# Kernel tuning notes

Hardware: AMD Instinct MI355X
Metric: run time of the kernel (lower is better)

Reference implementation:

```python
import jax, jax.numpy as jnp
import numpy as np

EMBED_DIM = 1024
NUM_HEADS = 16
D_K = EMBED_DIM // NUM_HEADS


def setup_inputs() -> dict:
    key = jax.random.key(0)
    ks = jax.random.split(key, 5)
    s = 1.0 / np.sqrt(EMBED_DIM)  # roughly match nn.Linear init scale
    return {
        "x": jax.random.normal(ks[0], (2, 2048, EMBED_DIM), dtype=jnp.float32),
        "wq": jax.random.normal(ks[1], (EMBED_DIM, EMBED_DIM), dtype=jnp.float32) * s,
        "wk": jax.random.normal(ks[2], (EMBED_DIM, EMBED_DIM), dtype=jnp.float32) * s,
        "wv": jax.random.normal(ks[3], (EMBED_DIM, EMBED_DIM), dtype=jnp.float32) * s,
        "wo": jax.random.normal(ks[4], (EMBED_DIM, EMBED_DIM), dtype=jnp.float32) * s,
    }


def reference(x, wq, wk, wv, wo):
    b, s, e = x.shape
    # nn.Linear(bias=False): y = x @ W.T
    def split_heads(t):
        return t.reshape(b, s, NUM_HEADS, D_K).transpose(0, 2, 1, 3)  # [b,h,s,d]
    q = split_heads(x @ wq.T)
    k = split_heads(x @ wk.T)
    v = split_heads(x @ wv.T)
    scores = jnp.einsum("bhqd,bhkd->bhqk", q, k) / jnp.sqrt(jnp.float32(D_K))
    attn = jax.nn.softmax(scores, axis=-1)
    out = jnp.einsum("bhqk,bhkd->bhqd", attn, v)  # [b,h,s,d]
    out = out.transpose(0, 2, 1, 3).reshape(b, s, e)
    return out @ wo.T
```

## Files before the change

### kernel.cpp

```cpp
#include <hip/hip_runtime.h>
#include <stdint.h>

typedef unsigned short u16;
typedef float f32x4 __attribute__((ext_vector_type(4)));
typedef __bf16 bf16x8 __attribute__((ext_vector_type(8)));
typedef short s16x4 __attribute__((ext_vector_type(4)));

__device__ __forceinline__ u16 f2bf(float f) {
  union { float f; uint32_t u; } c; c.f = f;
  uint32_t u = c.u;
  u += 0x7fffu + ((u >> 16) & 1u);
  return (u16)(u >> 16);
}

__device__ __forceinline__ uint32_t pkbf(float a, float b) {
  union { float f; uint32_t u; } ua, ub; ua.f = a; ub.f = b;
  return __builtin_amdgcn_perm(ub.u, ua.u, 0x07060302u);
}

#define GLOAD_LDS16(g, l)                                                              \
  __builtin_amdgcn_global_load_lds((__attribute__((address_space(1))) void*)(g),       \
                                   (__attribute__((address_space(3))) void*)(l), 16, 0, 0)

__global__ __launch_bounds__(256) void cvt_all(const float* __restrict__ x,
                                               const float* __restrict__ wq,
                                               const float* __restrict__ wk,
                                               const float* __restrict__ wv,
                                               const float* __restrict__ wo,
                                               u16* __restrict__ xb,
                                               u16* __restrict__ wqkvb,
                                               u16* __restrict__ wob) {
  int bx = blockIdx.x;
  const float* src;
  u16* dst;
  int i;
  if (bx < 4096) {
    src = x; dst = xb; i = bx * 256 + threadIdx.x;
  } else {
    int r = bx - 4096;
    int w = r >> 10;
    i = (r & 1023) * 256 + threadIdx.x;
    if (w == 0)      { src = wq; dst = wqkvb; }
    else if (w == 1) { src = wk; dst = wqkvb + 1048576; }
    else if (w == 2) { src = wv; dst = wqkvb + 2097152; }
    else             { src = wo; dst = wob; }
  }
  const float4 v = ((const float4*)src)[i];
  ushort4 o;
  o.x = f2bf(v.x); o.y = f2bf(v.y); o.z = f2bf(v.z); o.w = f2bf(v.w);
  ((ushort4*)dst)[i] = o;
}

__global__ __launch_bounds__(256, 3) void gemm_qkv(const u16* __restrict__ A,
                                                   const u16* __restrict__ B,
                                                   u16* __restrict__ QKb,
                                                   u16* __restrict__ Vt) {
  const int K = 1024;
  __shared__ __align__(16) u16 sA[3 * 4096];
  __shared__ __align__(16) u16 sB[3 * 4096];
  const int tid = threadIdx.x;
  const int lane = tid & 63;
  const int wave = tid >> 6;
  const int quad = lane >> 4, l16 = lane & 15;
  const int wm = (wave >> 1) * 64, wn = (wave & 1) * 64;
  const int bm = blockIdx.y * 128, bn = blockIdx.x * 128;

  f32x4 acc[4][4];
#pragma unroll
  for (int i = 0; i < 4; i++)
#pragma unroll
    for (int j = 0; j < 4; j++) acc[i][j] = (f32x4){0.f, 0.f, 0.f, 0.f};

#define QKV_STAGE(t, bi)                                                           \
  {                                                                                \
    const int k0s = (t) * 32;                                                      \
    char* dA = (char*)(sA + (bi) * 4096);                                          \
    char* dB = (char*)(sB + (bi) * 4096);                                          \
    _Pragma("unroll")                                                              \
    for (int k2 = 0; k2 < 2; k2++) {                                               \
      int u = k2 * 256 + tid;                                                      \
      int row = u >> 2, c4 = (u & 3) ^ (row & 3);                                  \
      GLOAD_LDS16(A + (size_t)(bm + row) * K + k0s + c4 * 8, dA + u * 16);         \
      GLOAD_LDS16(B + (size_t)(bn + row) * K + k0s + c4 * 8, dB + u * 16);         \
    }                                                                              \
  }

  QKV_STAGE(0, 0);
  QKV_STAGE(1, 1);

  int cur = 0, stg = 2;
  for (int T = 0; T < 32; ++T) {
    if (T < 31) asm volatile("s_waitcnt vmcnt(4)" ::: "memory");
    else        asm volatile("s_waitcnt vmcnt(0)" ::: "memory");
    __builtin_amdgcn_s_barrier();
    asm volatile("" ::: "memory");
    if (T < 30) QKV_STAGE(T + 2, stg);

    const u16* cA = sA + cur * 4096;
    const u16* cB = sB + cur * 4096;
    bf16x8 af[4], bfr[4];
#pragma unroll
    for (int mt = 0; mt < 4; mt++) {
      int ra = wm + mt * 16 + l16;
      af[mt] = *(const bf16x8*)&cA[ra * 32 + ((quad ^ (ra & 3)) * 8)];
    }
#pragma unroll
    for (int nt = 0; nt < 4; nt++) {
      int rb = wn + nt * 16 + l16;
      bfr[nt] = *(const bf16x8*)&cB[rb * 32 + ((quad ^ (rb & 3)) * 8)];
    }
#pragma unroll
    for (int mt = 0; mt < 4; mt++)
#pragma unroll
      for (int nt = 0; nt < 4; nt++)
        acc[mt][nt] = __builtin_amdgcn_mfma_f32_16x16x32_bf16(af[mt], bfr[nt], acc[mt][nt], 0, 0, 0);

    cur = (cur == 2) ? 0 : cur + 1;
    stg = (stg == 2) ? 0 : stg + 1;
  }
#undef QKV_STAGE

  if (blockIdx.x < 16) {
    const float qs = (blockIdx.x < 8) ? 0.18033688011f : 1.0f;
#pragma unroll
    for (int mt = 0; mt < 4; mt++)
#pragma unroll
      for (int nt = 0; nt < 4; nt++)
#pragma unroll
        for (int r = 0; r < 4; r++) {
          int row = bm + wm + mt * 16 + quad * 4 + r;
          int col = bn + wn + nt * 16 + l16;
          QKb[(size_t)row * 2048 + col] = f2bf(acc[mt][nt][r] * qs);
        }
  } else {
#pragma unroll
    for (int mt = 0; mt < 4; mt++)
#pragma unroll
      for (int nt = 0; nt < 4; nt++) {
        int hd = (bn - 2048) + wn + nt * 16 + l16;
        int tok = bm + wm + mt * 16 + quad * 4;
        ushort4 o;
        o.x = f2bf(acc[mt][nt][0]);
        o.y = f2bf(acc[mt][nt][1]);
        o.z = f2bf(acc[mt][nt][2]);
        o.w = f2bf(acc[mt][nt][3]);
        *(ushort4*)&Vt[(size_t)hd * 4096 + tok] = o;
      }
  }
}

__global__ __launch_bounds__(512, 4) void attn_fwd(const u16* __restrict__ QKb,
                                                   const u16* __restrict__ Vt,
                                                   u16* __restrict__ O) {
  const int bx = blockIdx.x;
  const int qt = bx >> 5;
  const int h  = (bx >> 1) & 15;
  const int b  = bx & 1;
  const int tid = threadIdx.x;
  const int lane = tid & 63;
  const int wave = tid >> 6;
  const int wq = wave >> 1;
  const int wk = wave & 1;
  const int quad = lane >> 4, l16 = lane & 15;

  __shared__ __align__(16) u16 smem[36864];
  u16* sQ = smem;
  u16* sK = smem + 8192;
  u16* sV = smem + 20480;

  const int tok0 = b * 2048;
  const int q0 = qt * 128;
  const int colh = h * 64;

#pragma unroll
  for (int k2 = 0; k2 < 2; k2++) {
    int c = k2 * 512 + tid;
    int row = c >> 3, c8 = (c & 7) ^ (row & 7);
    GLOAD_LDS16(QKb + (size_t)(tok0 + q0 + row) * 2048 + colh + c8 * 8,
                (char*)sQ + c * 16);
  }
#pragma unroll
  for (int t = 0; t < 2; t++) {
    int c = tid;
    int row = c >> 3, c8 = (c & 7) ^ (row & 7);
    GLOAD_LDS16(QKb + (size_t)(tok0 + t * 64 + row) * 2048 + 1024 + colh + c8 * 8,
                (char*)(sK + t * 4096) + c * 16);
    GLOAD_LDS16(Vt + (size_t)(colh + row) * 4096 + tok0 + t * 64 + c8 * 8,
                (char*)(sV + t * 4096) + c * 16);
  }
  asm volatile("s_waitcnt vmcnt(4)" ::: "memory");
  __builtin_amdgcn_s_barrier();
  asm volatile("" ::: "memory");

  bf16x8 aq[2][2];
#pragma unroll
  for (int sub = 0; sub < 2; sub++)
#pragma unroll
    for (int kh = 0; kh < 2; kh++) {
      int rq = wq * 32 + sub * 16 + l16;
      aq[sub][kh] = *(const bf16x8*)&sQ[rq * 64 + (((kh * 4 + quad) ^ (rq & 7)) * 8)];
    }

  f32x4 oacc[2][4];
  float lsum[2];
#pragma unroll
  for (int sub = 0; sub < 2; sub++) {
    lsum[sub] = 0.f;
#pragma unroll
    for (int db = 0; db < 4; db++) oacc[sub][db] = (f32x4){0.f, 0.f, 0.f, 0.f};
  }

  int kc = 0, stg3 = 2;

#define ITER_LOAD(IT, SS)                                                            \
  {                                                                                  \
    asm volatile("s_waitcnt lgkmcnt(0)" ::: "memory");                               \
    if ((IT) < 31) asm volatile("s_waitcnt vmcnt(2)" ::: "memory");                  \
    else           asm volatile("s_waitcnt vmcnt(0)" ::: "memory");                  \
    __builtin_amdgcn_s_barrier();                                                    \
    asm volatile("" ::: "memory");                                                   \
    if ((IT) < 30) {                                                                 \
      const int nkv = ((IT) + 2) * 64;                                               \
      int c = tid;                                                                   \
      int row = c >> 3, c8 = (c & 7) ^ (row & 7);                                    \
      GLOAD_LDS16(QKb + (size_t)(tok0 + nkv + row) * 2048 + 1024 + colh + c8 * 8,    \
                  (char*)(sK + stg3 * 4096) + c * 16);                               \
      GLOAD_LDS16(Vt + (size_t)(colh + row) * 4096 + tok0 + nkv + c8 * 8,            \
                  (char*)(sV + (((IT) + 2) & 3) * 4096) + c * 16);                   \
    }                                                                                \
    const u16* sKc = sK + kc * 4096;                                                 \
    bf16x8 kf[2][2];                                                                 \
    _Pragma("unroll")                                                                \
    for (int nt = 0; nt < 2; nt++)                                                   \
      _Pragma("unroll")                                                              \
      for (int kh = 0; kh < 2; kh++) {                                               \
        int rr = wk * 32 + nt * 16 + l16;                                            \
        kf[nt][kh] = *(const bf16x8*)&sKc[rr * 64 + (((kh * 4 + quad) ^ (rr & 7)) * 8)]; \
      }                                                                              \
    _Pragma("unroll")                                                                \
    for (int sub = 0; sub < 2; sub++)                                                \
      _Pragma("unroll")                                                              \
      for (int nt = 0; nt < 2; nt++) {                                               \
        f32x4 c0 = (f32x4){0.f, 0.f, 0.f, 0.f};                                      \
        c0 = __builtin_amdgcn_mfma_f32_16x16x32_bf16(kf[nt][0], aq[sub][0], c0, 0, 0, 0); \
        SS[sub][nt] = __builtin_amdgcn_mfma_f32_16x16x32_bf16(kf[nt][1], aq[sub][1], c0, 0, 0, 0); \
      }                                                                              \
    kc = (kc == 2) ? 0 : kc + 1;                                                     \
    stg3 = (stg3 == 2) ? 0 : stg3 + 1;                                               \
  }

#define ITER_SOFT(TT, SS)                                                            \
  {                                                                                  \
    const u16* sVp = sV + ((TT) & 3) * 4096;                                         \
    _Pragma("unroll")                                                                \
    for (int nt = 0; nt < 2; nt++) {                                                 \
      s16x4 vf[4];                                                                   \
      _Pragma("unroll")                                                              \
      for (int db = 0; db < 4; db++) {                                               \
        int row = db * 16 + l16;                                                     \
        int c16 = ((wk * 2 + nt) * 2 + (quad >> 1)) ^ (row & 7);                     \
        vf[db] = *(const s16x4*)&sVp[row * 64 + c16 * 8 + (quad & 1) * 4];           \
      }                                                                              \
      _Pragma("unroll")                                                              \
      for (int sub = 0; sub < 2; sub++) {                                            \
        f32x4 cS = SS[sub][nt];                                                      \
        float e0 = __builtin_amdgcn_exp2f(cS[0]);                                    \
        float e1 = __builtin_amdgcn_exp2f(cS[1]);                                    \
        float e2 = __builtin_amdgcn_exp2f(cS[2]);                                    \
        float e3 = __builtin_amdgcn_exp2f(cS[3]);                                    \
        lsum[sub] += (e0 + e1) + (e2 + e3);                                          \
        union { uint32_t u[2]; s16x4 v; } bb;                                        \
        bb.u[0] = pkbf(e0, e1);                                                      \
        bb.u[1] = pkbf(e2, e3);                                                      \
        _Pragma("unroll")                                                            \
        for (int db = 0; db < 4; db++)                                               \
          oacc[sub][db] = __builtin_amdgcn_mfma_f32_16x16x16bf16_1k(vf[db], bb.v, oacc[sub][db], 0, 0, 0); \
      }                                                                              \
    }                                                                                \
  }

  f32x4 SA[2][2], SB[2][2];
  ITER_LOAD(0, SA);
  for (int it = 1; it < 31; it += 2) {
    ITER_LOAD(it, SB);
    ITER_SOFT(it - 1, SA);
    ITER_LOAD(it + 1, SA);
    ITER_SOFT(it, SB);
  }
  ITER_LOAD(31, SB);
  ITER_SOFT(30, SA);
  ITER_SOFT(31, SB);
#undef ITER_LOAD
#undef ITER_SOFT

  asm volatile("s_waitcnt lgkmcnt(0)" ::: "memory");
  __builtin_amdgcn_s_barrier();

#pragma unroll
  for (int sub = 0; sub < 2; sub++) {
    float v = lsum[sub];
    v += __shfl_xor(v, 16, 64);
    v += __shfl_xor(v, 32, 64);
    lsum[sub] = v;
  }

  float* Rbase = (float*)smem + wq * 2048;
  float* lsumT = (float*)((char*)smem + 32768);

  if (wk == 0) {
#pragma unroll
    for (int sub = 0; sub < 2; sub++) {
#pragma unroll
      for (int db = 0; db < 4; db++) {
        int q = sub * 16 + l16;
        int d = db * 16 + quad * 4;
        *(f32x4*)&Rbase[q * 64 + (d ^ ((q & 7) << 3))] = oacc[sub][db];
      }
      if (quad == 0) lsumT[wq * 32 + sub * 16 + l16] = lsum[sub];
    }
  }
  __builtin_amdgcn_s_barrier();
  if (wk == 1) {
#pragma unroll
    for (int sub = 0; sub < 2; sub++) {
      int q = sub * 16 + l16;
      float rt = 1.0f / (lsum[sub] + lsumT[wq * 32 + q]);
#pragma unroll
      for (int db = 0; db < 4; db++) {
        int d = db * 16 + quad * 4;
        f32x4 o = *(const f32x4*)&Rbase[q * 64 + (d ^ ((q & 7) << 3))] + oacc[sub][db];
        ushort4 st;
        st.x = f2bf(o[0] * rt);
        st.y = f2bf(o[1] * rt);
        st.z = f2bf(o[2] * rt);
        st.w = f2bf(o[3] * rt);
        *(ushort4*)&O[(size_t)(tok0 + q0 + wq * 32 + q) * 1024 + colh + d] = st;
      }
    }
  }
}

__global__ __launch_bounds__(256, 2) void gemm_out(const u16* __restrict__ A,
                                                   const u16* __restrict__ B,
                                                   float* __restrict__ C) {
  const int N = 1024, K = 1024;
  __shared__ __align__(16) u16 sA[3 * 8192];
  __shared__ __align__(16) u16 sB[3 * 4096];
  const int tid = threadIdx.x;
  const int lane = tid & 63;
  const int wave = tid >> 6;
  const int quad = lane >> 4, l16 = lane & 15;
  const int wm = (wave >> 1) * 64, wn = (wave & 1) * 32;
  const int bm = blockIdx.y * 128, bn = blockIdx.x * 64;

  f32x4 acc[4][2];
#pragma unroll
  for (int i = 0; i < 4; i++)
#pragma unroll
    for (int j = 0; j < 2; j++) acc[i][j] = (f32x4){0.f, 0.f, 0.f, 0.f};

#define OUT_STAGE(t, bi)                                                           \
  {                                                                                \
    const int k0s = (t) * 64;                                                      \
    char* dA = (char*)(sA + (bi) * 8192);                                          \
    char* dB = (char*)(sB + (bi) * 4096);                                          \
    _Pragma("unroll")                                                              \
    for (int k2 = 0; k2 < 4; k2++) {                                               \
      int u = k2 * 256 + tid;                                                      \
      int row = u >> 3, c8 = (u & 7) ^ (row & 7);                                  \
      GLOAD_LDS16(A + (size_t)(bm + row) * K + k0s + c8 * 8, dA + u * 16);         \
    }                                                                              \
    _Pragma("unroll")                                                              \
    for (int k2 = 0; k2 < 2; k2++) {                                               \
      int u = k2 * 256 + tid;                                                      \
      int row = u >> 3, c8 = (u & 7) ^ (row & 7);                                  \
      GLOAD_LDS16(B + (size_t)(bn + row) * K + k0s + c8 * 8, dB + u * 16);         \
    }                                                                              \
  }

  OUT_STAGE(0, 0);
  OUT_STAGE(1, 1);

  int cur = 0, stg = 2;
  for (int T = 0; T < 16; ++T) {
    if (T < 15) asm volatile("s_waitcnt vmcnt(6)" ::: "memory");
    else        asm volatile("s_waitcnt vmcnt(0)" ::: "memory");
    __builtin_amdgcn_s_barrier();
    asm volatile("" ::: "memory");
    if (T < 14) OUT_STAGE(T + 2, stg);

    const u16* cA = sA + cur * 8192;
    const u16* cB = sB + cur * 4096;
    bf16x8 af[4][2], bfr[2][2];
#pragma unroll
    for (int mt = 0; mt < 4; mt++)
#pragma unroll
      for (int kh = 0; kh < 2; kh++) {
        int ra = wm + mt * 16 + l16;
        af[mt][kh] = *(const bf16x8*)&cA[ra * 64 + (((kh * 4 + quad) ^ (ra & 7)) * 8)];
      }
#pragma unroll
    for (int nt = 0; nt < 2; nt++)
#pragma unroll
      for (int kh = 0; kh < 2; kh++) {
        int rb = wn + nt * 16 + l16;
        bfr[nt][kh] = *(const bf16x8*)&cB[rb * 64 + (((kh * 4 + quad) ^ (rb & 7)) * 8)];
      }
#pragma unroll
    for (int mt = 0; mt < 4; mt++)
#pragma unroll
      for (int nt = 0; nt < 2; nt++) {
        acc[mt][nt] = __builtin_amdgcn_mfma_f32_16x16x32_bf16(af[mt][0], bfr[nt][0], acc[mt][nt], 0, 0, 0);
        acc[mt][nt] = __builtin_amdgcn_mfma_f32_16x16x32_bf16(af[mt][1], bfr[nt][1], acc[mt][nt], 0, 0, 0);
      }
    cur = (cur == 2) ? 0 : cur + 1;
    stg = (stg == 2) ? 0 : stg + 1;
  }
#undef OUT_STAGE

#pragma unroll
  for (int mt = 0; mt < 4; mt++)
#pragma unroll
    for (int nt = 0; nt < 2; nt++)
#pragma unroll
      for (int r = 0; r < 4; r++) {
        int row = bm + wm + mt * 16 + quad * 4 + r;
        int col = bn + wn + nt * 16 + l16;
        C[(size_t)row * N + col] = acc[mt][nt][r];
      }
}

extern "C" void kernel_launch(void* const* d_in, const int* in_sizes, int n_in,
                              void* d_out, int out_size, void* d_ws, size_t ws_size,
                              hipStream_t stream) {
  const float* x  = (const float*)d_in[0];
  const float* wq = (const float*)d_in[1];
  const float* wk = (const float*)d_in[2];
  const float* wv = (const float*)d_in[3];
  const float* wo = (const float*)d_in[4];
  float* out = (float*)d_out;
  char* ws = (char*)d_ws;
  const size_t MB = 1u << 20;

  u16* xb    = (u16*)(ws);
  u16* wqkvb = (u16*)(ws + 8 * MB);
  u16* wob   = (u16*)(ws + 14 * MB);
  u16* QKb   = (u16*)(ws + 16 * MB);
  u16* Vtb   = (u16*)(ws + 32 * MB);
  u16* Ob    = xb;

  cvt_all<<<8192, 256, 0, stream>>>(x, wq, wk, wv, wo, xb, wqkvb, wob);

  gemm_qkv<<<dim3(24, 32), 256, 0, stream>>>(xb, wqkvb, QKb, Vtb);

  attn_fwd<<<512, 512, 0, stream>>>(QKb, Vtb, Ob);

  gemm_out<<<dim3(16, 32), 256, 0, stream>>>(Ob, wob, out);
}
```

Measured before the change: 176.3 us.

## Switch attention kernel MFMAs from 16x16 tiles to 32x32x16 bf16

Rewrites the attention inner loops so that each wave computes a 32x32 score tile with four 32x32x16 MFMAs, and accumulates P·V with 32x32x16 MFMAs into two 16-wide accumulators. The aim is fewer MFMA issues and fewer LDS fragment loads per tile. In exchange, the probability operand must be rearranged across the two half-waves with lane shuffles, and the epilogue indexing changes to match the 32x32 output layout. This adds shuffle overhead and accumulator register pressure.

After: 176.7 us. About the same (+0.3%).

```diff
diff --git a/kernel.cpp b/kernel.cpp
--- a/kernel.cpp
+++ b/kernel.cpp
@@ -3,6 +3,7 @@
 
 typedef unsigned short u16;
 typedef float f32x4 __attribute__((ext_vector_type(4)));
+typedef float f32x16 __attribute__((ext_vector_type(16)));
 typedef __bf16 bf16x8 __attribute__((ext_vector_type(8)));
 typedef short s16x4 __attribute__((ext_vector_type(4)));
 
@@ -161,7 +162,8 @@
   const int wave = tid >> 6;
   const int wq = wave >> 1;
   const int wk = wave & 1;
-  const int quad = lane >> 4, l16 = lane & 15;
+  const int l32 = lane & 31;
+  const int hh = lane >> 5;
 
   __shared__ __align__(16) u16 smem[36864];
   u16* sQ = smem;
@@ -192,23 +194,18 @@
   __builtin_amdgcn_s_barrier();
   asm volatile("" ::: "memory");
 
-  bf16x8 aq[2][2];
-#pragma unroll
-  for (int sub = 0; sub < 2; sub++)
-#pragma unroll
-    for (int kh = 0; kh < 2; kh++) {
-      int rq = wq * 32 + sub * 16 + l16;
-      aq[sub][kh] = *(const bf16x8*)&sQ[rq * 64 + (((kh * 4 + quad) ^ (rq & 7)) * 8)];
-    }
-
-  f32x4 oacc[2][4];
-  float lsum[2];
-#pragma unroll
-  for (int sub = 0; sub < 2; sub++) {
-    lsum[sub] = 0.f;
-#pragma unroll
-    for (int db = 0; db < 4; db++) oacc[sub][db] = (f32x4){0.f, 0.f, 0.f, 0.f};
-  }
+  bf16x8 aq[4];
+#pragma unroll
+  for (int win = 0; win < 4; win++) {
+    int rq = wq * 32 + l32;
+    int ch = win * 2 + hh;
+    aq[win] = *(const bf16x8*)&sQ[rq * 64 + ((ch ^ (rq & 7)) * 8)];
+  }
+
+  f32x16 oacc[2];
+  float lsum = 0.f;
+#pragma unroll
+  for (int j = 0; j < 16; j++) { oacc[0][j] = 0.f; oacc[1][j] = 0.f; }
 
   int kc = 0, stg3 = 2;
 
@@ -229,22 +226,18 @@
                   (char*)(sV + (((IT) + 2) & 3) * 4096) + c * 16);                   \
     }                                                                                \
     const u16* sKc = sK + kc * 4096;                                                 \
-    bf16x8 kf[2][2];                                                                 \
+    bf16x8 kf[4];                                                                    \
     _Pragma("unroll")                                                                \
-    for (int nt = 0; nt < 2; nt++)                                                   \
-      _Pragma("unroll")                                                              \
-      for (int kh = 0; kh < 2; kh++) {                                               \
-        int rr = wk * 32 + nt * 16 + l16;                                            \
-        kf[nt][kh] = *(const bf16x8*)&sKc[rr * 64 + (((kh * 4 + quad) ^ (rr & 7)) * 8)]; \
-      }                                                                              \
+    for (int win = 0; win < 4; win++) {                                              \
+      int rk = wk * 32 + l32;                                                        \
+      int ch = win * 2 + hh;                                                         \
+      kf[win] = *(const bf16x8*)&sKc[rk * 64 + ((ch ^ (rk & 7)) * 8)];               \
+    }                                                                                \
     _Pragma("unroll")                                                                \
-    for (int sub = 0; sub < 2; sub++)                                                \
-      _Pragma("unroll")                                                              \
-      for (int nt = 0; nt < 2; nt++) {                                               \
-        f32x4 c0 = (f32x4){0.f, 0.f, 0.f, 0.f};                                      \
-        c0 = __builtin_amdgcn_mfma_f32_16x16x32_bf16(kf[nt][0], aq[sub][0], c0, 0, 0, 0); \
-        SS[sub][nt] = __builtin_amdgcn_mfma_f32_16x16x32_bf16(kf[nt][1], aq[sub][1], c0, 0, 0, 0); \
-      }                                                                              \
+    for (int j = 0; j < 16; j++) SS[j] = 0.f;                                        \
+    _Pragma("unroll")                                                                \
+    for (int win = 0; win < 4; win++)                                                \
+      SS = __builtin_amdgcn_mfma_f32_32x32x16_bf16(kf[win], aq[win], SS, 0, 0, 0);   \
     kc = (kc == 2) ? 0 : kc + 1;                                                     \
     stg3 = (stg3 == 2) ? 0 : stg3 + 1;                                               \
   }
@@ -252,34 +245,44 @@
 #define ITER_SOFT(TT, SS)                                                            \
   {                                                                                  \
     const u16* sVp = sV + ((TT) & 3) * 4096;                                         \
+    bf16x8 vf[2][2];                                                                 \
     _Pragma("unroll")                                                                \
-    for (int nt = 0; nt < 2; nt++) {                                                 \
-      s16x4 vf[4];                                                                   \
+    for (int dt = 0; dt < 2; dt++)                                                   \
       _Pragma("unroll")                                                              \
-      for (int db = 0; db < 4; db++) {                                               \
-        int row = db * 16 + l16;                                                     \
-        int c16 = ((wk * 2 + nt) * 2 + (quad >> 1)) ^ (row & 7);                     \
-        vf[db] = *(const s16x4*)&sVp[row * 64 + c16 * 8 + (quad & 1) * 4];           \
+      for (int win = 0; win < 2; win++) {                                            \
+        int row = dt * 32 + l32;                                                     \
+        int ch = wk * 4 + win * 2 + hh;                                              \
+        vf[dt][win] = *(const bf16x8*)&sVp[row * 64 + ((ch ^ (row & 7)) * 8)];       \
       }                                                                              \
+    _Pragma("unroll")                                                                \
+    for (int win = 0; win < 2; win++) {                                              \
+      float e0 = __builtin_amdgcn_exp2f(SS[win * 8 + 0]);                            \
+      float e1 = __builtin_amdgcn_exp2f(SS[win * 8 + 1]);                            \
+      float e2 = __builtin_amdgcn_exp2f(SS[win * 8 + 2]);                            \
+      float e3 = __builtin_amdgcn_exp2f(SS[win * 8 + 3]);                            \
+      float e4 = __builtin_amdgcn_exp2f(SS[win * 8 + 4]);                            \
+      float e5 = __builtin_amdgcn_exp2f(SS[win * 8 + 5]);                            \
+      float e6 = __builtin_amdgcn_exp2f(SS[win * 8 + 6]);                            \
+      float e7 = __builtin_amdgcn_exp2f(SS[win * 8 + 7]);                            \
+      lsum += ((e0 + e1) + (e2 + e3)) + ((e4 + e5) + (e6 + e7));                     \
+      uint32_t d0 = pkbf(e0, e1), d1 = pkbf(e2, e3);                                 \
+      uint32_t d2 = pkbf(e4, e5), d3 = pkbf(e6, e7);                                 \
+      uint32_t x0 = (uint32_t)__shfl_xor((int)d0, 32);                               \
+      uint32_t x1 = (uint32_t)__shfl_xor((int)d1, 32);                               \
+      uint32_t x2 = (uint32_t)__shfl_xor((int)d2, 32);                               \
+      uint32_t x3 = (uint32_t)__shfl_xor((int)d3, 32);                               \
+      union { uint32_t u[4]; bf16x8 v; } Bf;                                         \
+      Bf.u[0] = hh ? x2 : d0;                                                        \
+      Bf.u[1] = hh ? x3 : d1;                                                        \
+      Bf.u[2] = hh ? d2 : x0;                                                        \
+      Bf.u[3] = hh ? d3 : x1;                                                        \
       _Pragma("unroll")                                                              \
-      for (int sub = 0; sub < 2; sub++) {                                            \
-        f32x4 cS = SS[sub][nt];                                                      \
-        float e0 = __builtin_amdgcn_exp2f(cS[0]);                                    \
-        float e1 = __builtin_amdgcn_exp2f(cS[1]);                                    \
-        float e2 = __builtin_amdgcn_exp2f(cS[2]);                                    \
-        float e3 = __builtin_amdgcn_exp2f(cS[3]);                                    \
-        lsum[sub] += (e0 + e1) + (e2 + e3);                                          \
-        union { uint32_t u[2]; s16x4 v; } bb;                                        \
-        bb.u[0] = pkbf(e0, e1);                                                      \
-        bb.u[1] = pkbf(e2, e3);                                                      \
-        _Pragma("unroll")                                                            \
-        for (int db = 0; db < 4; db++)                                               \
-          oacc[sub][db] = __builtin_amdgcn_mfma_f32_16x16x16bf16_1k(vf[db], bb.v, oacc[sub][db], 0, 0, 0); \
-      }                                                                              \
+      for (int dt = 0; dt < 2; dt++)                                                 \
+        oacc[dt] = __builtin_amdgcn_mfma_f32_32x32x16_bf16(vf[dt][win], Bf.v, oacc[dt], 0, 0, 0); \
     }                                                                                \
   }
 
-  f32x4 SA[2][2], SB[2][2];
+  f32x16 SA, SB;
   ITER_LOAD(0, SA);
   for (int it = 1; it < 31; it += 2) {
     ITER_LOAD(it, SB);
@@ -296,47 +299,47 @@
   asm volatile("s_waitcnt lgkmcnt(0)" ::: "memory");
   __builtin_amdgcn_s_barrier();
 
-#pragma unroll
-  for (int sub = 0; sub < 2; sub++) {
-    float v = lsum[sub];
-    v += __shfl_xor(v, 16, 64);
-    v += __shfl_xor(v, 32, 64);
-    lsum[sub] = v;
-  }
+  float lsum_tot = lsum + __shfl_xor(lsum, 32);
 
   float* Rbase = (float*)smem + wq * 2048;
   float* lsumT = (float*)((char*)smem + 32768);
 
   if (wk == 0) {
 #pragma unroll
-    for (int sub = 0; sub < 2; sub++) {
-#pragma unroll
-      for (int db = 0; db < 4; db++) {
-        int q = sub * 16 + l16;
-        int d = db * 16 + quad * 4;
-        *(f32x4*)&Rbase[q * 64 + (d ^ ((q & 7) << 3))] = oacc[sub][db];
-      }
-      if (quad == 0) lsumT[wq * 32 + sub * 16 + l16] = lsum[sub];
-    }
+    for (int dt = 0; dt < 2; dt++)
+#pragma unroll
+      for (int g = 0; g < 4; g++) {
+        int d = dt * 32 + 8 * g + 4 * hh;
+        f32x4 v;
+        v[0] = oacc[dt][4 * g + 0];
+        v[1] = oacc[dt][4 * g + 1];
+        v[2] = oacc[dt][4 * g + 2];
+        v[3] = oacc[dt][4 * g + 3];
+        *(f32x4*)&Rbase[l32 * 64 + (d ^ ((l32 & 7) << 3))] = v;
+      }
+    if (hh == 0) lsumT[wq * 32 + l32] = lsum_tot;
   }
   __builtin_amdgcn_s_barrier();
   if (wk == 1) {
-#pragma unroll
-    for (int sub = 0; sub < 2; sub++) {
-      int q = sub * 16 + l16;
-      float rt = 1.0f / (lsum[sub] + lsumT[wq * 32 + q]);
-#pragma unroll
-      for (int db = 0; db < 4; db++) {
-        int d = db * 16 + quad * 4;
-        f32x4 o = *(const f32x4*)&Rbase[q * 64 + (d ^ ((q & 7) << 3))] + oacc[sub][db];
+    float rt = 1.0f / (lsum_tot + lsumT[wq * 32 + l32]);
+#pragma unroll
+    for (int dt = 0; dt < 2; dt++)
+#pragma unroll
+      for (int g = 0; g < 4; g++) {
+        int d = dt * 32 + 8 * g + 4 * hh;
+        int loc = l32 * 64 + (d ^ ((l32 & 7) << 3));
+        f32x4 o = *(const f32x4*)&Rbase[loc];
+        o[0] += oacc[dt][4 * g + 0];
+        o[1] += oacc[dt][4 * g + 1];
+        o[2] += oacc[dt][4 * g + 2];
+        o[3] += oacc[dt][4 * g + 3];
         ushort4 st;
         st.x = f2bf(o[0] * rt);
         st.y = f2bf(o[1] * rt);
         st.z = f2bf(o[2] * rt);
         st.w = f2bf(o[3] * rt);
-        *(ushort4*)&O[(size_t)(tok0 + q0 + wq * 32 + q) * 1024 + colh + d] = st;
-      }
-    }
+        *(ushort4*)&O[(size_t)(tok0 + q0 + wq * 32 + l32) * 1024 + colh + d] = st;
+      }
   }
 }
 
```
